# Performance work log

Hardware: AMD Instinct MI355X
Metric: run time of the kernel (lower is better)

The kernel has to match this reference:

```python
import jax, jax.numpy as jnp
import numpy as np

UNITS = 1024

def setup_inputs() -> dict:
    key = jax.random.key(0)
    k1, k2, k3 = jax.random.split(key, 3)
    B, T, F = 32, 512, 1024
    scale_g = 1.0 / np.sqrt(F + UNITS)
    return {
        "inputs": jax.random.normal(k1, (B, T, F), dtype=jnp.float32),
        "gate_kernel": jax.random.normal(k2, (F + UNITS, 2 * UNITS), dtype=jnp.float32) * scale_g,
        "gate_bias": jnp.ones((2 * UNITS,), dtype=jnp.float32),  # TF GRUCell default gate bias = 1.0
        "cand_kernel": jax.random.normal(k3, (F + UNITS, UNITS), dtype=jnp.float32) * scale_g,
        "cand_bias": jnp.zeros((UNITS,), dtype=jnp.float32),
    }

def _gru_step(x, h, gate_kernel, gate_bias, cand_kernel, cand_bias):
    # TF GRUCell math: gates from [x, h], candidate from [x, r*h]
    xh = jnp.concatenate([x, h], axis=-1)                      # [B, F+U]
    gates = jax.nn.sigmoid(xh @ gate_kernel + gate_bias)       # [B, 2U]
    r, u = jnp.split(gates, 2, axis=-1)
    xrh = jnp.concatenate([x, r * h], axis=-1)
    c = jnp.tanh(xrh @ cand_kernel + cand_bias)                # [B, U]
    return u * h + (1.0 - u) * c

def reference(inputs, gate_kernel, gate_bias, cand_kernel, cand_bias):
    B = inputs.shape[0]
    h0 = jnp.zeros((B, UNITS), dtype=jnp.float32)  # cell.zero_state
    xs = jnp.swapaxes(inputs, 0, 1)                # [T, B, F] (unstack over time)

    def step(h, x):
        h_new = _gru_step(x, h, gate_kernel, gate_bias, cand_kernel, cand_bias)
        return h_new, h_new  # GRU output == new state

    _, ys = jax.lax.scan(step, h0, xs)             # ys: [T, B, U]
    return jnp.swapaxes(ys, 0, 1)                  # stack on axis=1 -> [B, T, U]
```

## Files before the change

### kernel.cpp

```cpp
#include <hip/hip_runtime.h>
#include <math.h>

#define BB 32
#define TT 512
#define FF 1024
#define UU 1024
#define NBLK 64

typedef __attribute__((ext_vector_type(8))) short s8v;
typedef __attribute__((ext_vector_type(4))) float f4v;
typedef __attribute__((ext_vector_type(2))) float f2v;
typedef __attribute__((ext_vector_type(2))) unsigned int u2v;

static __device__ __forceinline__ unsigned short f2bf(float f) {
    unsigned int u = __builtin_bit_cast(unsigned int, f);
    u += 0x7fff + ((u >> 16) & 1);
    return (unsigned short)(u >> 16);
}
static __device__ __forceinline__ float bf2f(unsigned short b) {
    unsigned int u = ((unsigned int)b) << 16;
    return __builtin_bit_cast(float, u);
}

static __device__ __forceinline__ s8v ld_b128_sc(const void* p) {
    s8v r;
    asm volatile("global_load_dwordx4 %0, %1, off sc0 sc1" : "=v"(r) : "v"(p));
    return r;
}
static __device__ __forceinline__ f4v ld_f128_sc(const void* p) {
    f4v r;
    asm volatile("global_load_dwordx4 %0, %1, off sc0 sc1" : "=v"(r) : "v"(p));
    return r;
}
static __device__ __forceinline__ f2v ld_f64_sc(const void* p) {
    f2v r;
    asm volatile("global_load_dwordx2 %0, %1, off sc0 sc1" : "=v"(r) : "v"(p));
    return r;
}
static __device__ __forceinline__ void st_b128_sc(void* p, f4v v) {
    asm volatile("global_store_dwordx4 %0, %1, off sc0 sc1" :: "v"(p), "v"(v));
}
static __device__ __forceinline__ void st_b64_sc(void* p, u2v v) {
    asm volatile("global_store_dwordx2 %0, %1, off sc0 sc1" :: "v"(p), "v"(v));
}
static __device__ __forceinline__ void st_f64_sc(void* p, f2v v) {
    asm volatile("global_store_dwordx2 %0, %1, off sc0 sc1" :: "v"(p), "v"(v));
}
static __device__ __forceinline__ void st_b32_sc(void* p, unsigned int v) {
    asm volatile("global_store_dword %0, %1, off sc0 sc1" :: "v"(p), "v"(v));
}
static __device__ __forceinline__ void vm_drain_schedfence() {
    asm volatile("s_waitcnt vmcnt(0)" ::: "memory");
    __builtin_amdgcn_sched_barrier(0);
}

__global__ __launch_bounds__(256) void cvt_bf16(
    const float* __restrict__ in, unsigned short* __restrict__ out, int n4)
{
    int i = blockIdx.x * 256 + threadIdx.x;
    if (i < n4) {
        float4 v = ((const float4*)in)[i];
        ushort4 o;
        o.x = f2bf(v.x); o.y = f2bf(v.y); o.z = f2bf(v.z); o.w = f2bf(v.w);
        ((ushort4*)out)[i] = o;
    }
}

template<int ROWS, int COLS>
__global__ __launch_bounds__(256) void transpose_bf16(
    const float* __restrict__ W, unsigned short* __restrict__ WT)
{
    __shared__ float tl[32][33];
    const int tx = threadIdx.x, ty = threadIdx.y;
    const int bx = blockIdx.x, by = blockIdx.y;
    #pragma unroll
    for (int i = 0; i < 4; ++i) {
        int r = by * 32 + ty + i * 8;
        int c = bx * 32 + tx;
        tl[ty + i * 8][tx] = W[(size_t)r * COLS + c];
    }
    __syncthreads();
    #pragma unroll
    for (int i = 0; i < 4; ++i) {
        int n = bx * 32 + ty + i * 8;
        int k = by * 32 + tx;
        WT[(size_t)n * ROWS + k] = f2bf(tl[tx][ty + i * 8]);
    }
}

__global__ __launch_bounds__(256) void gemm_xproj(
    const unsigned short* __restrict__ A,
    const unsigned short* __restrict__ BT,
    unsigned short* __restrict__ C,
    int N)
{
    __shared__ unsigned short Al[128][72];
    __shared__ unsigned short Bl[128][72];
    const int tid  = threadIdx.x;
    const int lane = tid & 63;
    const int wave = tid >> 6;
    const int l15  = lane & 15;
    const int kg   = lane >> 4;
    const int m0   = blockIdx.y * 128;
    const int n0   = blockIdx.x * 128;
    const int rowOff = (wave >> 1) * 64;
    const int colOff = (wave & 1) * 64;

    f4v acc[4][4];
    #pragma unroll
    for (int m = 0; m < 4; ++m)
        #pragma unroll
        for (int n = 0; n < 4; ++n) acc[m][n] = (f4v){0.f, 0.f, 0.f, 0.f};

    for (int k0 = 0; k0 < 1024; k0 += 64) {
        #pragma unroll
        for (int it = 0; it < 4; ++it) {
            int c = tid + it * 256;
            int r = c >> 3, off = (c & 7) * 8;
            *(s8v*)&Al[r][off] = *(const s8v*)(A + (size_t)(m0 + r) * 1024 + k0 + off);
            *(s8v*)&Bl[r][off] = *(const s8v*)(BT + (size_t)(n0 + r) * 2048 + k0 + off);
        }
        __syncthreads();
        #pragma unroll
        for (int ks = 0; ks < 2; ++ks) {
            s8v a[4], b[4];
            #pragma unroll
            for (int m = 0; m < 4; ++m)
                a[m] = *(const s8v*)&Al[rowOff + m * 16 + l15][ks * 32 + kg * 8];
            #pragma unroll
            for (int n = 0; n < 4; ++n)
                b[n] = *(const s8v*)&Bl[colOff + n * 16 + l15][ks * 32 + kg * 8];
            #pragma unroll
            for (int m = 0; m < 4; ++m)
                #pragma unroll
                for (int n = 0; n < 4; ++n)
                    acc[m][n] = __builtin_amdgcn_mfma_f32_16x16x32_bf16(a[m], b[n], acc[m][n], 0, 0, 0);
        }
        __syncthreads();
    }
    #pragma unroll
    for (int m = 0; m < 4; ++m)
        #pragma unroll
        for (int n = 0; n < 4; ++n)
            #pragma unroll
            for (int i = 0; i < 4; ++i) {
                int row = m0 + rowOff + m * 16 + kg * 4 + i;
                int col = n0 + colOff + n * 16 + l15;
                C[(size_t)row * N + col] = f2bf(acc[m][n][i]);
            }
}

__device__ __forceinline__ void grid_barrier(unsigned* counter, unsigned target, int tid)
{
    asm volatile("s_waitcnt vmcnt(0)" ::: "memory");
    __syncthreads();
    if (tid == 0) {
        __hip_atomic_fetch_add(counter, 1u, __ATOMIC_RELAXED, __HIP_MEMORY_SCOPE_AGENT);
        while (__hip_atomic_load(counter, __ATOMIC_RELAXED, __HIP_MEMORY_SCOPE_AGENT) < target)
            __builtin_amdgcn_s_sleep(1);
    }
    __syncthreads();
}

__global__ __launch_bounds__(256, 1) void gru_persistent(
    const unsigned short* __restrict__ WgT,
    const unsigned short* __restrict__ WcT,
    const unsigned short* __restrict__ Xgb,
    const unsigned short* __restrict__ Xcb,
    const float* __restrict__ bg,
    const float* __restrict__ bc,
    float* __restrict__ h,
    unsigned short* __restrict__ hb,
    unsigned short* __restrict__ rhb,
    float* __restrict__ ub,
    float* __restrict__ out,
    unsigned* __restrict__ bar)
{
    __shared__ float red[4][32][32];
    __shared__ unsigned short wc_l[16 * 1024];
    const int tid  = threadIdx.x;
    const int lane = tid & 63;
    const int wave = tid >> 6;
    const int l15  = lane & 15;
    const int kg   = lane >> 4;
    const int blk  = blockIdx.x;
    const int gj0  = blk * 32;
    const int cj0  = blk * 16;
    const int kb   = wave * 256;
    const bool is_r = (gj0 < UU);

    #pragma unroll
    for (int it = 0; it < 8; ++it) {
        int c   = tid + it * 256;
        int col = c >> 7;
        int k   = (c & 127) * 8;
        s8v w = *(const s8v*)(WcT + (size_t)(cj0 + col) * 2048 + 1024 + k);
        *(s8v*)&wc_l[col * 1024 + (k ^ ((col & 7) << 3))] = w;
    }

    s8v bgf[2][8];
    #pragma unroll
    for (int n = 0; n < 2; ++n)
        #pragma unroll
        for (int kk = 0; kk < 8; ++kk)
            bgf[n][kk] = *(const s8v*)(WgT + (size_t)(gj0 + n * 16 + l15) * 2048
                                            + 1024 + kb + kk * 32 + kg * 8);

    const int eb = tid >> 3;
    const int eq = tid & 7;
    const float4 bgv = *(const float4*)(bg + gj0 + eq * 4);
    const float2 bcv = *(const float2*)(bc + cj0 + eq * 2);

    __syncthreads();

    unsigned epoch = 0;
    ushort4 xg = *(const ushort4*)(Xgb + ((size_t)eb * TT + 0) * 2048 + gj0 + eq * 4);

    for (int t = 0; t < TT; ++t) {
        f4v hsl = (f4v){0.f,0.f,0.f,0.f};
        if (is_r) hsl = ld_f128_sc(h + eb * UU + gj0 + eq * 4);

        s8v a[2][8];
        #pragma unroll
        for (int m = 0; m < 2; ++m)
            #pragma unroll
            for (int kk = 0; kk < 8; ++kk)
                a[m][kk] = ld_b128_sc(hb + (size_t)(m * 16 + l15) * 1024 + kb + kk * 32 + kg * 8);
        vm_drain_schedfence();

        f4v acc[2][2];
        #pragma unroll
        for (int m = 0; m < 2; ++m)
            #pragma unroll
            for (int n = 0; n < 2; ++n) acc[m][n] = (f4v){0.f, 0.f, 0.f, 0.f};
        #pragma unroll
        for (int kk = 0; kk < 8; ++kk)
            #pragma unroll
            for (int m = 0; m < 2; ++m)
                #pragma unroll
                for (int n = 0; n < 2; ++n)
                    acc[m][n] = __builtin_amdgcn_mfma_f32_16x16x32_bf16(a[m][kk], bgf[n][kk], acc[m][n], 0, 0, 0);

        #pragma unroll
        for (int m = 0; m < 2; ++m)
            #pragma unroll
            for (int n = 0; n < 2; ++n)
                #pragma unroll
                for (int i = 0; i < 4; ++i)
                    red[wave][m * 16 + kg * 4 + i][n * 16 + l15] = acc[m][n][i];
        __syncthreads();

        f4v pre = *(const f4v*)&red[0][eb][eq * 4];
        #pragma unroll
        for (int w = 1; w < 4; ++w) pre += *(const f4v*)&red[w][eb][eq * 4];
        pre[0] += bf2f(xg.x) + bgv.x;
        pre[1] += bf2f(xg.y) + bgv.y;
        pre[2] += bf2f(xg.z) + bgv.z;
        pre[3] += bf2f(xg.w) + bgv.w;
        float s0 = 1.f / (1.f + __expf(-pre[0]));
        float s1 = 1.f / (1.f + __expf(-pre[1]));
        float s2 = 1.f / (1.f + __expf(-pre[2]));
        float s3 = 1.f / (1.f + __expf(-pre[3]));
        if (is_r) {
            unsigned int lo = (unsigned int)f2bf(s0 * hsl[0]) | ((unsigned int)f2bf(s1 * hsl[1]) << 16);
            unsigned int hi = (unsigned int)f2bf(s2 * hsl[2]) | ((unsigned int)f2bf(s3 * hsl[3]) << 16);
            st_b64_sc(rhb + eb * UU + gj0 + eq * 4, (u2v){lo, hi});
        } else {
            st_b128_sc(ub + eb * UU + (gj0 - UU) + eq * 4, (f4v){s0, s1, s2, s3});
        }

        ushort2 xc = *(const ushort2*)(Xcb + ((size_t)eb * TT + t) * 1024 + cj0 + eq * 2);
        f2v hv = ld_f64_sc(h + eb * UU + cj0 + eq * 2);

        ++epoch;
        grid_barrier(bar, epoch * NBLK, tid);

        f2v uv = ld_f64_sc(ub + eb * UU + cj0 + eq * 2);

        s8v ac[2][8];
        #pragma unroll
        for (int m = 0; m < 2; ++m)
            #pragma unroll
            for (int kk = 0; kk < 8; ++kk)
                ac[m][kk] = ld_b128_sc(rhb + (size_t)(m * 16 + l15) * 1024 + kb + kk * 32 + kg * 8);
        vm_drain_schedfence();

        f4v acc2[2];
        acc2[0] = (f4v){0.f, 0.f, 0.f, 0.f};
        acc2[1] = (f4v){0.f, 0.f, 0.f, 0.f};
        #pragma unroll
        for (int kk = 0; kk < 8; ++kk) {
            s8v bcf = *(const s8v*)&wc_l[l15 * 1024 + ((kb + kk * 32 + kg * 8) ^ ((l15 & 7) << 3))];
            #pragma unroll
            for (int m = 0; m < 2; ++m)
                acc2[m] = __builtin_amdgcn_mfma_f32_16x16x32_bf16(ac[m][kk], bcf, acc2[m], 0, 0, 0);
        }

        float* redc = (float*)red;
        #pragma unroll
        for (int m = 0; m < 2; ++m)
            #pragma unroll
            for (int i = 0; i < 4; ++i)
                redc[((size_t)wave * 32 + m * 16 + kg * 4 + i) * 16 + l15] = acc2[m][i];
        __syncthreads();

        float2 pre2 = *(const float2*)&redc[(0 * 32 + eb) * 16 + eq * 2];
        #pragma unroll
        for (int w = 1; w < 4; ++w) {
            float2 p = *(const float2*)&redc[((size_t)w * 32 + eb) * 16 + eq * 2];
            pre2.x += p.x; pre2.y += p.y;
        }
        float c0 = pre2.x + bf2f(xc.x) + bcv.x;
        float c1 = pre2.y + bf2f(xc.y) + bcv.y;
        c0 = fminf(fmaxf(c0, -15.f), 15.f);
        c1 = fminf(fmaxf(c1, -15.f), 15.f);
        float e0 = __expf(2.f * c0), e1 = __expf(2.f * c1);
        float t0 = (e0 - 1.f) / (e0 + 1.f);
        float t1 = (e1 - 1.f) / (e1 + 1.f);
        float hn0 = uv[0] * hv[0] + (1.f - uv[0]) * t0;
        float hn1 = uv[1] * hv[1] + (1.f - uv[1]) * t1;

        st_f64_sc(h + eb * UU + cj0 + eq * 2, (f2v){hn0, hn1});
        st_b32_sc(hb + eb * UU + cj0 + eq * 2,
                  (unsigned int)f2bf(hn0) | ((unsigned int)f2bf(hn1) << 16));
        *(float2*)(out + ((size_t)eb * TT + t) * UU + cj0 + eq * 2) = make_float2(hn0, hn1);

        if (t + 1 < TT)
            xg = *(const ushort4*)(Xgb + ((size_t)eb * TT + t + 1) * 2048 + gj0 + eq * 4);

        ++epoch;
        if (t + 1 < TT) grid_barrier(bar, epoch * NBLK, tid);
    }
}

__global__ __launch_bounds__(256) void gru_gates2(
    const unsigned short* __restrict__ hb, const unsigned short* __restrict__ WgT,
    const unsigned short* __restrict__ Xgb, const float* __restrict__ bg,
    const float* __restrict__ h, unsigned short* __restrict__ rhb,
    float* __restrict__ ubuf, int t)
{
    __shared__ unsigned short hb_l[32][1032];
    __shared__ unsigned short Wl[16][1032];
    __shared__ float red[4][32][16];
    const int tid = threadIdx.x, lane = tid & 63, wave = tid >> 6;
    const int l15 = lane & 15, kg = lane >> 4;
    const int j0 = blockIdx.x * 16;
    #pragma unroll
    for (int it = 0; it < 16; ++it) {
        int c = tid + it * 256; int r = c >> 7, off = (c & 127) * 8;
        *(s8v*)&hb_l[r][off] = *(const s8v*)(hb + (size_t)r * 1024 + off);
    }
    #pragma unroll
    for (int it = 0; it < 8; ++it) {
        int c = tid + it * 256; int r = c >> 7, off = (c & 127) * 8;
        *(s8v*)&Wl[r][off] = *(const s8v*)(WgT + (size_t)(j0 + r) * 2048 + 1024 + off);
    }
    __syncthreads();
    f4v acc0 = (f4v){0.f,0.f,0.f,0.f}, acc1 = (f4v){0.f,0.f,0.f,0.f};
    const int kbase = wave * 256;
    #pragma unroll
    for (int kk = 0; kk < 8; ++kk) {
        int k = kbase + kk * 32 + kg * 8;
        s8v a0 = *(const s8v*)&hb_l[l15][k];
        s8v a1 = *(const s8v*)&hb_l[16 + l15][k];
        s8v b  = *(const s8v*)&Wl[l15][k];
        acc0 = __builtin_amdgcn_mfma_f32_16x16x32_bf16(a0, b, acc0, 0, 0, 0);
        acc1 = __builtin_amdgcn_mfma_f32_16x16x32_bf16(a1, b, acc1, 0, 0, 0);
    }
    #pragma unroll
    for (int i = 0; i < 4; ++i) {
        red[wave][kg * 4 + i][l15] = acc0[i];
        red[wave][16 + kg * 4 + i][l15] = acc1[i];
    }
    __syncthreads();
    for (int e = tid; e < 512; e += 256) {
        int b = e >> 4, col = e & 15;
        int j = j0 + col;
        float pre = red[0][b][col] + red[1][b][col] + red[2][b][col] + red[3][b][col];
        pre += bf2f(Xgb[((size_t)b * TT + t) * 2048 + j]) + bg[j];
        float s = 1.f / (1.f + __expf(-pre));
        if (j < UU) rhb[b * UU + j] = f2bf(s * h[b * UU + j]);
        else        ubuf[b * UU + (j - UU)] = s;
    }
}

__global__ __launch_bounds__(256) void gru_cand2(
    const unsigned short* __restrict__ rhb, const unsigned short* __restrict__ WcT,
    const unsigned short* __restrict__ Xcb, const float* __restrict__ bc,
    const float* __restrict__ ubuf, float* __restrict__ h,
    unsigned short* __restrict__ hb, float* __restrict__ out, int t)
{
    __shared__ unsigned short rh_l[32][1032];
    __shared__ unsigned short Wl[16][1032];
    __shared__ float red[4][32][16];
    const int tid = threadIdx.x, lane = tid & 63, wave = tid >> 6;
    const int l15 = lane & 15, kg = lane >> 4;
    const int j0 = blockIdx.x * 16;
    #pragma unroll
    for (int it = 0; it < 16; ++it) {
        int c = tid + it * 256; int r = c >> 7, off = (c & 127) * 8;
        *(s8v*)&rh_l[r][off] = *(const s8v*)(rhb + (size_t)r * 1024 + off);
    }
    #pragma unroll
    for (int it = 0; it < 8; ++it) {
        int c = tid + it * 256; int r = c >> 7, off = (c & 127) * 8;
        *(s8v*)&Wl[r][off] = *(const s8v*)(WcT + (size_t)(j0 + r) * 2048 + 1024 + off);
    }
    __syncthreads();
    f4v acc0 = (f4v){0.f,0.f,0.f,0.f}, acc1 = (f4v){0.f,0.f,0.f,0.f};
    const int kbase = wave * 256;
    #pragma unroll
    for (int kk = 0; kk < 8; ++kk) {
        int k = kbase + kk * 32 + kg * 8;
        s8v a0 = *(const s8v*)&rh_l[l15][k];
        s8v a1 = *(const s8v*)&rh_l[16 + l15][k];
        s8v b  = *(const s8v*)&Wl[l15][k];
        acc0 = __builtin_amdgcn_mfma_f32_16x16x32_bf16(a0, b, acc0, 0, 0, 0);
        acc1 = __builtin_amdgcn_mfma_f32_16x16x32_bf16(a1, b, acc1, 0, 0, 0);
    }
    #pragma unroll
    for (int i = 0; i < 4; ++i) {
        red[wave][kg * 4 + i][l15] = acc0[i];
        red[wave][16 + kg * 4 + i][l15] = acc1[i];
    }
    __syncthreads();
    for (int e = tid; e < 512; e += 256) {
        int b = e >> 4, col = e & 15;
        int j = j0 + col;
        float pre = red[0][b][col] + red[1][b][col] + red[2][b][col] + red[3][b][col];
        pre += bf2f(Xcb[((size_t)b * TT + t) * 1024 + j]) + bc[j];
        float cv = tanhf(pre);
        float u  = ubuf[b * UU + j];
        float hv = h[b * UU + j];
        float hn = u * hv + (1.f - u) * cv;
        h[b * UU + j]  = hn;
        hb[b * UU + j] = f2bf(hn);
        out[((size_t)b * TT + t) * UU + j] = hn;
    }
}

extern "C" void kernel_launch(void* const* d_in, const int* in_sizes, int n_in,
                              void* d_out, int out_size, void* d_ws, size_t ws_size,
                              hipStream_t stream) {
    const float* x  = (const float*)d_in[0];
    const float* Wg = (const float*)d_in[1];
    const float* bg = (const float*)d_in[2];
    const float* Wc = (const float*)d_in[3];
    const float* bc = (const float*)d_in[4];
    float* out = (float*)d_out;

    const size_t XB_B  = (size_t)BB * TT * FF * 2;
    const size_t WGT_B = (size_t)2 * UU * (FF + UU) * 2;
    const size_t WCT_B = (size_t)UU * (FF + UU) * 2;
    const size_t XG_B  = (size_t)BB * TT * 2 * UU * 2;
    const size_t XC_B  = (size_t)BB * TT * UU * 2;
    const size_t H_B   = (size_t)BB * UU * 4;
    const size_t HB_B  = (size_t)BB * UU * 2;
    const size_t BAR_B = 256;
    const size_t NEED  = XB_B + WGT_B + WCT_B + XG_B + XC_B + H_B + HB_B * 2 + H_B + BAR_B;

    char* p = (char*)d_ws;
    unsigned short* xb  = (unsigned short*)p;            p += XB_B;
    unsigned short* WgT = (unsigned short*)p;            p += WGT_B;
    unsigned short* WcT = (unsigned short*)p;            p += WCT_B;
    unsigned short* Xgb = (unsigned short*)p;            p += XG_B;
    unsigned short* Xcb = (unsigned short*)p;            p += XC_B;
    float*          h   = (float*)p;                     p += H_B;
    unsigned short* hb  = (unsigned short*)p;            p += HB_B;
    unsigned short* rhb = (unsigned short*)p;            p += HB_B;
    float*          ub  = (float*)p;                     p += H_B;
    unsigned*       bar = (unsigned*)p;                  p += BAR_B;

    cvt_bf16<<<(BB * TT * FF / 4 + 255) / 256, 256, 0, stream>>>(x, xb, BB * TT * FF / 4);
    transpose_bf16<FF + UU, 2 * UU><<<dim3(64, 64), dim3(32, 8), 0, stream>>>(Wg, WgT);
    transpose_bf16<FF + UU, UU>    <<<dim3(32, 64), dim3(32, 8), 0, stream>>>(Wc, WcT);
    gemm_xproj<<<dim3(2 * UU / 128, BB * TT / 128), 256, 0, stream>>>(xb, WgT, Xgb, 2 * UU);
    gemm_xproj<<<dim3(UU / 128,     BB * TT / 128), 256, 0, stream>>>(xb, WcT, Xcb, UU);
    hipMemsetAsync(h,   0, H_B,   stream);
    hipMemsetAsync(hb,  0, HB_B,  stream);
    hipMemsetAsync(bar, 0, BAR_B, stream);

    if (ws_size >= NEED) {
        gru_persistent<<<NBLK, 256, 0, stream>>>(WgT, WcT, Xgb, Xcb, bg, bc,
                                                 h, hb, rhb, ub, out, bar);
    } else {
        for (int t = 0; t < TT; ++t) {
            gru_gates2<<<128, 256, 0, stream>>>(hb, WgT, Xgb, bg, h, rhb, ub, t);
            gru_cand2 <<< 64, 256, 0, stream>>>(rhb, WcT, Xcb, bc, ub, h, hb, out, t);
        }
    }
}
```

Before: 4.774 ms.

## Replace flat grid barrier with per-XCD hierarchical barrier and co-locate r/u gates

The persistent GRU kernel is relaunched with 512 blocks. Each block registers itself on its XCD through an atomic counter, and only the first 8 per XCD stay active, which pins 8 workers to each XCD. The single global atomic barrier becomes a two-level barrier: a local counter per XCD, with only the last arriver touching the global counter and releasing the others through a local flag. Each block now computes both the r and u gates for the same 16 columns, so u and h stay in registers, and the gate projection is stored interleaved so one load fetches both. The aim is to cut cross-XCD barrier latency and remove the ub/h global round trips, at the cost of relying on the hardware XCC_ID register and on enough blocks being scheduled to every XCD.

```diff
diff --git a/kernel.cpp b/kernel.cpp
--- a/kernel.cpp
+++ b/kernel.cpp
@@ -5,12 +5,10 @@
 #define TT 512
 #define FF 1024
 #define UU 1024
-#define NBLK 64
+#define GRID 512
 
 typedef __attribute__((ext_vector_type(8))) short s8v;
 typedef __attribute__((ext_vector_type(4))) float f4v;
-typedef __attribute__((ext_vector_type(2))) float f2v;
-typedef __attribute__((ext_vector_type(2))) unsigned int u2v;
 
 static __device__ __forceinline__ unsigned short f2bf(float f) {
     unsigned int u = __builtin_bit_cast(unsigned int, f);
@@ -27,27 +25,22 @@
     asm volatile("global_load_dwordx4 %0, %1, off sc0 sc1" : "=v"(r) : "v"(p));
     return r;
 }
-static __device__ __forceinline__ f4v ld_f128_sc(const void* p) {
-    f4v r;
-    asm volatile("global_load_dwordx4 %0, %1, off sc0 sc1" : "=v"(r) : "v"(p));
-    return r;
-}
-static __device__ __forceinline__ f2v ld_f64_sc(const void* p) {
-    f2v r;
-    asm volatile("global_load_dwordx2 %0, %1, off sc0 sc1" : "=v"(r) : "v"(p));
-    return r;
-}
-static __device__ __forceinline__ void st_b128_sc(void* p, f4v v) {
-    asm volatile("global_store_dwordx4 %0, %1, off sc0 sc1" :: "v"(p), "v"(v));
-}
-static __device__ __forceinline__ void st_b64_sc(void* p, u2v v) {
-    asm volatile("global_store_dwordx2 %0, %1, off sc0 sc1" :: "v"(p), "v"(v));
-}
-static __device__ __forceinline__ void st_f64_sc(void* p, f2v v) {
-    asm volatile("global_store_dwordx2 %0, %1, off sc0 sc1" :: "v"(p), "v"(v));
-}
 static __device__ __forceinline__ void st_b32_sc(void* p, unsigned int v) {
     asm volatile("global_store_dword %0, %1, off sc0 sc1" :: "v"(p), "v"(v));
+}
+static __device__ __forceinline__ s8v ld_b128_pin(const void* p) {
+    s8v r;
+    asm volatile("global_load_dwordx4 %0, %1, off" : "=v"(r) : "v"(p));
+    return r;
+}
+static __device__ __forceinline__ unsigned atom_add_ret_l2(unsigned* p, unsigned v) {
+    unsigned old;
+    asm volatile("global_atomic_add %0, %1, %2, off sc0\n\ts_waitcnt vmcnt(0)"
+                 : "=v"(old) : "v"(p), "v"(v) : "memory");
+    return old;
+}
+static __device__ __forceinline__ void atom_add_l2(unsigned* p, unsigned v) {
+    asm volatile("global_atomic_add %0, %1, off" :: "v"(p), "v"(v) : "memory");
 }
 static __device__ __forceinline__ void vm_drain_schedfence() {
     asm volatile("s_waitcnt vmcnt(0)" ::: "memory");
@@ -88,6 +81,7 @@
     }
 }
 
+template<bool INTERLEAVE>
 __global__ __launch_bounds__(256) void gemm_xproj(
     const unsigned short* __restrict__ A,
     const unsigned short* __restrict__ BT,
@@ -146,79 +140,99 @@
             for (int i = 0; i < 4; ++i) {
                 int row = m0 + rowOff + m * 16 + kg * 4 + i;
                 int col = n0 + colOff + n * 16 + l15;
-                C[(size_t)row * N + col] = f2bf(acc[m][n][i]);
+                size_t off = INTERLEAVE
+                    ? (size_t)row * N + ((col < 1024) ? col * 2 : (col - 1024) * 2 + 1)
+                    : (size_t)row * N + col;
+                C[off] = f2bf(acc[m][n][i]);
             }
 }
 
-__device__ __forceinline__ void grid_barrier(unsigned* counter, unsigned target, int tid)
-{
-    asm volatile("s_waitcnt vmcnt(0)" ::: "memory");
-    __syncthreads();
-    if (tid == 0) {
-        __hip_atomic_fetch_add(counter, 1u, __ATOMIC_RELAXED, __HIP_MEMORY_SCOPE_AGENT);
-        while (__hip_atomic_load(counter, __ATOMIC_RELAXED, __HIP_MEMORY_SCOPE_AGENT) < target)
-            __builtin_amdgcn_s_sleep(1);
-    }
-    __syncthreads();
-}
-
-__global__ __launch_bounds__(256, 1) void gru_persistent(
+__global__ __launch_bounds__(256, 2) void gru_hier(
     const unsigned short* __restrict__ WgT,
     const unsigned short* __restrict__ WcT,
-    const unsigned short* __restrict__ Xgb,
+    const unsigned short* __restrict__ Xg2,
     const unsigned short* __restrict__ Xcb,
     const float* __restrict__ bg,
     const float* __restrict__ bc,
-    float* __restrict__ h,
     unsigned short* __restrict__ hb,
     unsigned short* __restrict__ rhb,
-    float* __restrict__ ub,
     float* __restrict__ out,
     unsigned* __restrict__ bar)
 {
-    __shared__ float red[4][32][32];
+    __shared__ float redg[4][32][32];
     __shared__ unsigned short wc_l[16 * 1024];
+    __shared__ int rank_sh;
     const int tid  = threadIdx.x;
     const int lane = tid & 63;
     const int wave = tid >> 6;
     const int l15  = lane & 15;
     const int kg   = lane >> 4;
-    const int blk  = blockIdx.x;
-    const int gj0  = blk * 32;
-    const int cj0  = blk * 16;
-    const int kb   = wave * 256;
-    const bool is_r = (gj0 < UU);
+
+    int xcd;
+    asm volatile("s_getreg_b32 %0, hwreg(HW_REG_XCC_ID)" : "=s"(xcd));
+    xcd &= 7;
+    unsigned* lcnt = bar + 64  + xcd * 32;
+    unsigned* lgo  = bar + 384 + xcd * 32;
+    unsigned* lreg = bar + 704 + xcd * 32;
+    unsigned* gcnt = bar;
+
+    if (tid == 0) rank_sh = (int)atom_add_ret_l2(lreg, 1u);
+    __syncthreads();
+    const int rank = rank_sh;
+    if (rank >= 8) return;
+    const int w = xcd * 8 + rank;
+    const int J = w * 16;
 
     #pragma unroll
     for (int it = 0; it < 8; ++it) {
         int c   = tid + it * 256;
         int col = c >> 7;
         int k   = (c & 127) * 8;
-        s8v w = *(const s8v*)(WcT + (size_t)(cj0 + col) * 2048 + 1024 + k);
-        *(s8v*)&wc_l[col * 1024 + (k ^ ((col & 7) << 3))] = w;
-    }
-
+        s8v wv = *(const s8v*)(WcT + (size_t)(J + col) * 2048 + 1024 + k);
+        *(s8v*)&wc_l[col * 1024 + (k ^ ((col & 7) << 3))] = wv;
+    }
+    const int kb = wave * 256;
     s8v bgf[2][8];
     #pragma unroll
-    for (int n = 0; n < 2; ++n)
-        #pragma unroll
-        for (int kk = 0; kk < 8; ++kk)
-            bgf[n][kk] = *(const s8v*)(WgT + (size_t)(gj0 + n * 16 + l15) * 2048
-                                            + 1024 + kb + kk * 32 + kg * 8);
-
-    const int eb = tid >> 3;
-    const int eq = tid & 7;
-    const float4 bgv = *(const float4*)(bg + gj0 + eq * 4);
-    const float2 bcv = *(const float2*)(bc + cj0 + eq * 2);
-
-    __syncthreads();
-
-    unsigned epoch = 0;
-    ushort4 xg = *(const ushort4*)(Xgb + ((size_t)eb * TT + 0) * 2048 + gj0 + eq * 4);
+    for (int kk = 0; kk < 8; ++kk) {
+        bgf[0][kk] = ld_b128_pin(WgT + (size_t)(J + l15) * 2048 + 1024 + kb + kk * 32 + kg * 8);
+        bgf[1][kk] = ld_b128_pin(WgT + (size_t)(1024 + J + l15) * 2048 + 1024 + kb + kk * 32 + kg * 8);
+    }
+    vm_drain_schedfence();
+
+    const int b  = tid >> 3;
+    const int c0 = (tid & 7) * 2;
+    const float2 bgr = { bg[J + c0],        bg[J + c0 + 1] };
+    const float2 bgu = { bg[1024 + J + c0], bg[1024 + J + c0 + 1] };
+    const float2 bcp = { bc[J + c0],        bc[J + c0 + 1] };
+
+    __syncthreads();
+
+    auto hbar = [&](unsigned ph) {
+        asm volatile("s_waitcnt vmcnt(0)" ::: "memory");
+        __syncthreads();
+        if (tid == 0) {
+            unsigned old = atom_add_ret_l2(lcnt, 1u);
+            if (((old + 1) & 7) == 0) {
+                __hip_atomic_fetch_add(gcnt, 1u, __ATOMIC_RELAXED, __HIP_MEMORY_SCOPE_AGENT);
+                while (__hip_atomic_load(gcnt, __ATOMIC_RELAXED, __HIP_MEMORY_SCOPE_AGENT) < 8u * ph)
+                    __builtin_amdgcn_s_sleep(1);
+                atom_add_l2(lgo, 1u);
+            } else {
+                while (atom_add_ret_l2(lgo, 0u) < ph)
+                    __builtin_amdgcn_s_sleep(1);
+            }
+        }
+        __syncthreads();
+    };
+
+    float h0 = 0.f, h1 = 0.f;
+    float u0 = 0.f, u1 = 0.f;
 
     for (int t = 0; t < TT; ++t) {
-        f4v hsl = (f4v){0.f,0.f,0.f,0.f};
-        if (is_r) hsl = ld_f128_sc(h + eb * UU + gj0 + eq * 4);
+        const size_t bt = (size_t)b * TT + t;
+        ushort4 xgp = *(const ushort4*)(Xg2 + bt * 2048 + (size_t)(J + c0) * 2);
+        unsigned xcp = *(const unsigned*)(Xcb + bt * 1024 + J + c0);
 
         s8v a[2][8];
         #pragma unroll
@@ -247,35 +261,28 @@
             for (int n = 0; n < 2; ++n)
                 #pragma unroll
                 for (int i = 0; i < 4; ++i)
-                    red[wave][m * 16 + kg * 4 + i][n * 16 + l15] = acc[m][n][i];
-        __syncthreads();
-
-        f4v pre = *(const f4v*)&red[0][eb][eq * 4];
-        #pragma unroll
-        for (int w = 1; w < 4; ++w) pre += *(const f4v*)&red[w][eb][eq * 4];
-        pre[0] += bf2f(xg.x) + bgv.x;
-        pre[1] += bf2f(xg.y) + bgv.y;
-        pre[2] += bf2f(xg.z) + bgv.z;
-        pre[3] += bf2f(xg.w) + bgv.w;
-        float s0 = 1.f / (1.f + __expf(-pre[0]));
-        float s1 = 1.f / (1.f + __expf(-pre[1]));
-        float s2 = 1.f / (1.f + __expf(-pre[2]));
-        float s3 = 1.f / (1.f + __expf(-pre[3]));
-        if (is_r) {
-            unsigned int lo = (unsigned int)f2bf(s0 * hsl[0]) | ((unsigned int)f2bf(s1 * hsl[1]) << 16);
-            unsigned int hi = (unsigned int)f2bf(s2 * hsl[2]) | ((unsigned int)f2bf(s3 * hsl[3]) << 16);
-            st_b64_sc(rhb + eb * UU + gj0 + eq * 4, (u2v){lo, hi});
-        } else {
-            st_b128_sc(ub + eb * UU + (gj0 - UU) + eq * 4, (f4v){s0, s1, s2, s3});
-        }
-
-        ushort2 xc = *(const ushort2*)(Xcb + ((size_t)eb * TT + t) * 1024 + cj0 + eq * 2);
-        f2v hv = ld_f64_sc(h + eb * UU + cj0 + eq * 2);
-
-        ++epoch;
-        grid_barrier(bar, epoch * NBLK, tid);
-
-        f2v uv = ld_f64_sc(ub + eb * UU + cj0 + eq * 2);
+                    redg[wave][m * 16 + kg * 4 + i][n * 16 + l15] = acc[m][n][i];
+        __syncthreads();
+
+        {
+            float2 pr = {0.f, 0.f}, pu = {0.f, 0.f};
+            #pragma unroll
+            for (int wv = 0; wv < 4; ++wv) {
+                float2 p = *(const float2*)&redg[wv][b][c0];
+                float2 q = *(const float2*)&redg[wv][b][16 + c0];
+                pr.x += p.x; pr.y += p.y;
+                pu.x += q.x; pu.y += q.y;
+            }
+            pr.x += bf2f(xgp.x) + bgr.x;  pu.x += bf2f(xgp.y) + bgu.x;
+            pr.y += bf2f(xgp.z) + bgr.y;  pu.y += bf2f(xgp.w) + bgu.y;
+            float r0 = 1.f / (1.f + __expf(-pr.x));
+            float r1 = 1.f / (1.f + __expf(-pr.y));
+            u0 = 1.f / (1.f + __expf(-pu.x));
+            u1 = 1.f / (1.f + __expf(-pu.y));
+            unsigned pk = (unsigned)f2bf(r0 * h0) | ((unsigned)f2bf(r1 * h1) << 16);
+            st_b32_sc(rhb + (size_t)b * 1024 + J + c0, pk);
+        }
+        hbar((unsigned)(2 * t + 1));
 
         s8v ac[2][8];
         #pragma unroll
@@ -290,13 +297,13 @@
         acc2[1] = (f4v){0.f, 0.f, 0.f, 0.f};
         #pragma unroll
         for (int kk = 0; kk < 8; ++kk) {
-            s8v bcf = *(const s8v*)&wc_l[l15 * 1024 + ((kb + kk * 32 + kg * 8) ^ ((l15 & 7) << 3))];
+            int k = kb + kk * 32 + kg * 8;
+            s8v bcf = *(const s8v*)&wc_l[l15 * 1024 + (k ^ ((l15 & 7) << 3))];
             #pragma unroll
             for (int m = 0; m < 2; ++m)
                 acc2[m] = __builtin_amdgcn_mfma_f32_16x16x32_bf16(ac[m][kk], bcf, acc2[m], 0, 0, 0);
         }
-
-        float* redc = (float*)red;
+        float* redc = (float*)redg;
         #pragma unroll
         for (int m = 0; m < 2; ++m)
             #pragma unroll
@@ -304,32 +311,27 @@
                 redc[((size_t)wave * 32 + m * 16 + kg * 4 + i) * 16 + l15] = acc2[m][i];
         __syncthreads();
 
-        float2 pre2 = *(const float2*)&redc[(0 * 32 + eb) * 16 + eq * 2];
-        #pragma unroll
-        for (int w = 1; w < 4; ++w) {
-            float2 p = *(const float2*)&redc[((size_t)w * 32 + eb) * 16 + eq * 2];
-            pre2.x += p.x; pre2.y += p.y;
-        }
-        float c0 = pre2.x + bf2f(xc.x) + bcv.x;
-        float c1 = pre2.y + bf2f(xc.y) + bcv.y;
-        c0 = fminf(fmaxf(c0, -15.f), 15.f);
-        c1 = fminf(fmaxf(c1, -15.f), 15.f);
-        float e0 = __expf(2.f * c0), e1 = __expf(2.f * c1);
-        float t0 = (e0 - 1.f) / (e0 + 1.f);
-        float t1 = (e1 - 1.f) / (e1 + 1.f);
-        float hn0 = uv[0] * hv[0] + (1.f - uv[0]) * t0;
-        float hn1 = uv[1] * hv[1] + (1.f - uv[1]) * t1;
-
-        st_f64_sc(h + eb * UU + cj0 + eq * 2, (f2v){hn0, hn1});
-        st_b32_sc(hb + eb * UU + cj0 + eq * 2,
-                  (unsigned int)f2bf(hn0) | ((unsigned int)f2bf(hn1) << 16));
-        *(float2*)(out + ((size_t)eb * TT + t) * UU + cj0 + eq * 2) = make_float2(hn0, hn1);
-
-        if (t + 1 < TT)
-            xg = *(const ushort4*)(Xgb + ((size_t)eb * TT + t + 1) * 2048 + gj0 + eq * 4);
-
-        ++epoch;
-        if (t + 1 < TT) grid_barrier(bar, epoch * NBLK, tid);
+        {
+            float2 pc = {0.f, 0.f};
+            #pragma unroll
+            for (int wv = 0; wv < 4; ++wv) {
+                float2 p = *(const float2*)&redc[((size_t)wv * 32 + b) * 16 + c0];
+                pc.x += p.x; pc.y += p.y;
+            }
+            float cv0 = pc.x + bf2f((unsigned short)(xcp & 0xffff)) + bcp.x;
+            float cv1 = pc.y + bf2f((unsigned short)(xcp >> 16)) + bcp.y;
+            cv0 = fminf(fmaxf(cv0, -15.f), 15.f);
+            cv1 = fminf(fmaxf(cv1, -15.f), 15.f);
+            float e0 = __expf(2.f * cv0), e1 = __expf(2.f * cv1);
+            float t0 = (e0 - 1.f) / (e0 + 1.f);
+            float t1 = (e1 - 1.f) / (e1 + 1.f);
+            h0 = u0 * h0 + (1.f - u0) * t0;
+            h1 = u1 * h1 + (1.f - u1) * t1;
+            st_b32_sc(hb + (size_t)b * 1024 + J + c0,
+                      (unsigned)f2bf(h0) | ((unsigned)f2bf(h1) << 16));
+            *(float2*)(out + bt * 1024 + J + c0) = make_float2(h0, h1);
+        }
+        hbar((unsigned)(2 * t + 2));
     }
 }
 
@@ -363,9 +365,9 @@
         int k = kbase + kk * 32 + kg * 8;
         s8v a0 = *(const s8v*)&hb_l[l15][k];
         s8v a1 = *(const s8v*)&hb_l[16 + l15][k];
-        s8v b  = *(const s8v*)&Wl[l15][k];
-        acc0 = __builtin_amdgcn_mfma_f32_16x16x32_bf16(a0, b, acc0, 0, 0, 0);
-        acc1 = __builtin_amdgcn_mfma_f32_16x16x32_bf16(a1, b, acc1, 0, 0, 0);
+        s8v bv = *(const s8v*)&Wl[l15][k];
+        acc0 = __builtin_amdgcn_mfma_f32_16x16x32_bf16(a0, bv, acc0, 0, 0, 0);
+        acc1 = __builtin_amdgcn_mfma_f32_16x16x32_bf16(a1, bv, acc1, 0, 0, 0);
     }
     #pragma unroll
     for (int i = 0; i < 4; ++i) {
@@ -414,9 +416,9 @@
         int k = kbase + kk * 32 + kg * 8;
         s8v a0 = *(const s8v*)&rh_l[l15][k];
         s8v a1 = *(const s8v*)&rh_l[16 + l15][k];
-        s8v b  = *(const s8v*)&Wl[l15][k];
-        acc0 = __builtin_amdgcn_mfma_f32_16x16x32_bf16(a0, b, acc0, 0, 0, 0);
-        acc1 = __builtin_amdgcn_mfma_f32_16x16x32_bf16(a1, b, acc1, 0, 0, 0);
+        s8v bv = *(const s8v*)&Wl[l15][k];
+        acc0 = __builtin_amdgcn_mfma_f32_16x16x32_bf16(a0, bv, acc0, 0, 0, 0);
+        acc1 = __builtin_amdgcn_mfma_f32_16x16x32_bf16(a1, bv, acc1, 0, 0, 0);
     }
     #pragma unroll
     for (int i = 0; i < 4; ++i) {
@@ -431,8 +433,8 @@
         pre += bf2f(Xcb[((size_t)b * TT + t) * 1024 + j]) + bc[j];
         float cv = tanhf(pre);
         float u  = ubuf[b * UU + j];
-        float hv = h[b * UU + j];
-        float hn = u * hv + (1.f - u) * cv;
+        float hvv = h[b * UU + j];
+        float hn = u * hvv + (1.f - u) * cv;
         h[b * UU + j]  = hn;
         hb[b * UU + j] = f2bf(hn);
         out[((size_t)b * TT + t) * UU + j] = hn;
@@ -456,7 +458,7 @@
     const size_t XC_B  = (size_t)BB * TT * UU * 2;
     const size_t H_B   = (size_t)BB * UU * 4;
     const size_t HB_B  = (size_t)BB * UU * 2;
-    const size_t BAR_B = 256;
+    const size_t BAR_B = 4096;
     const size_t NEED  = XB_B + WGT_B + WCT_B + XG_B + XC_B + H_B + HB_B * 2 + H_B + BAR_B;
 
     char* p = (char*)d_ws;
@@ -471,18 +473,23 @@
     float*          ub  = (float*)p;                     p += H_B;
     unsigned*       bar = (unsigned*)p;                  p += BAR_B;
 
+    const bool persistent = (ws_size >= NEED);
+
     cvt_bf16<<<(BB * TT * FF / 4 + 255) / 256, 256, 0, stream>>>(x, xb, BB * TT * FF / 4);
     transpose_bf16<FF + UU, 2 * UU><<<dim3(64, 64), dim3(32, 8), 0, stream>>>(Wg, WgT);
     transpose_bf16<FF + UU, UU>    <<<dim3(32, 64), dim3(32, 8), 0, stream>>>(Wc, WcT);
-    gemm_xproj<<<dim3(2 * UU / 128, BB * TT / 128), 256, 0, stream>>>(xb, WgT, Xgb, 2 * UU);
-    gemm_xproj<<<dim3(UU / 128,     BB * TT / 128), 256, 0, stream>>>(xb, WcT, Xcb, UU);
+    if (persistent)
+        gemm_xproj<true><<<dim3(2 * UU / 128, BB * TT / 128), 256, 0, stream>>>(xb, WgT, Xgb, 2 * UU);
+    else
+        gemm_xproj<false><<<dim3(2 * UU / 128, BB * TT / 128), 256, 0, stream>>>(xb, WgT, Xgb, 2 * UU);
+    gemm_xproj<false><<<dim3(UU / 128, BB * TT / 128), 256, 0, stream>>>(xb, WcT, Xcb, UU);
     hipMemsetAsync(h,   0, H_B,   stream);
     hipMemsetAsync(hb,  0, HB_B,  stream);
     hipMemsetAsync(bar, 0, BAR_B, stream);
 
-    if (ws_size >= NEED) {
-        gru_persistent<<<NBLK, 256, 0, stream>>>(WgT, WcT, Xgb, Xcb, bg, bc,
-                                                 h, hb, rhb, ub, out, bar);
+    if (persistent) {
+        gru_hier<<<GRID, 256, 0, stream>>>(WgT, WcT, Xgb, Xcb, bg, bc,
+                                           hb, rhb, out, bar);
     } else {
         for (int t = 0; t < TT; ++t) {
             gru_gates2<<<128, 256, 0, stream>>>(hb, WgT, Xgb, bg, h, rhb, ub, t);
```

After: 6.443 ms. +35.0%, slower.
